# Performance work log

Measured on AMD Instinct MI355X. Metric: run time of the kernel, lower is better.

## Reference

```python
import jax, jax.numpy as jnp
import numpy as np

N = 30000        # entities
R_EFF = 9        # 2*r+1 after enrich() with r=4
F_IN = 256       # insize
HID = 256        # hidden
NCLS = 32        # numcls
BASES = 16
E = 500000       # number of (enriched) triples / nonzeros


def setup_inputs() -> dict:
    key = jax.random.key(0)
    ks = jax.random.split(key, 8)
    features = jax.random.normal(ks[0], (N, F_IN), dtype=jnp.float32)
    # sparse vertical adjacency: entry at (rel*N + dst, src)
    ver_rows = jax.random.randint(ks[1], (E,), 0, R_EFF * N, dtype=jnp.int32)
    ver_cols = jax.random.randint(ks[2], (E,), 0, N, dtype=jnp.int32)
    # row-sum normalization (sum_sparse in the original): vals = 1 / row_degree
    deg = jax.ops.segment_sum(jnp.ones((E,), jnp.float32), ver_rows,
                              num_segments=R_EFF * N)
    ver_vals = 1.0 / deg[ver_rows]
    # xavier-uniform-ish params
    def xavier(k, shape):
        fan_in, fan_out = shape[-2], shape[-1]
        lim = jnp.sqrt(6.0 / (fan_in + fan_out)) * jnp.sqrt(2.0)  # relu gain
        return jax.random.uniform(k, shape, jnp.float32, -lim, lim)
    comps1 = xavier(ks[3], (R_EFF, BASES))
    bases1 = xavier(ks[4], (BASES, F_IN, HID))
    comps2 = xavier(ks[5], (R_EFF, BASES))
    bases2 = xavier(ks[6], (BASES, HID, NCLS))
    bias1 = jnp.zeros((HID,), jnp.float32)
    bias2 = jnp.zeros((NCLS,), jnp.float32)
    return {"features": features, "ver_vals": ver_vals,
            "comps1": comps1, "bases1": bases1,
            "comps2": comps2, "bases2": bases2,
            "bias1": bias1, "bias2": bias2,
            "ver_rows": ver_rows, "ver_cols": ver_cols}


def _spmm(vals, rows, cols, x, num_rows):
    # sparse [num_rows, n] @ x [n, d] -> [num_rows, d]
    msg = vals[:, None] * x[cols]          # (E, d) gather + scale
    return jax.ops.segment_sum(msg, rows, num_segments=num_rows)


def reference(features, ver_vals, comps1, bases1, comps2, bases2,
              bias1, bias2, ver_rows, ver_cols):
    n, f = features.shape
    r = comps1.shape[0]
    # layer 1: sparse aggregate, per-relation transform (basis decomp), sum over r
    h = _spmm(ver_vals, ver_rows, ver_cols, features, r * n)  # (r*n, f)
    h = h.reshape(r, n, f)
    w1 = jnp.einsum('rb,bfe->rfe', comps1, bases1)            # (r, f, hid)
    h = jnp.einsum('rnf,rfe->ne', h, w1)                      # bmm + sum over r
    h = jax.nn.relu(h + bias1)                                # (n, hid)
    # layer 2
    e = h.shape[1]
    h2 = _spmm(ver_vals, ver_rows, ver_cols, h, r * n).reshape(r, n, e)
    w2 = jnp.einsum('rb,bec->rec', comps2, bases2)            # (r, hid, ncls)
    out = jnp.einsum('rne,rec->nc', h2, w2) + bias2           # link_prediction=False
    return out
```

## Files before the change

### kernel.cpp

```cpp
#include <hip/hip_runtime.h>

typedef __attribute__((ext_vector_type(8))) short bf16x8;
typedef __attribute__((ext_vector_type(4))) float f32x4;

constexpr int NB = 16;
constexpr int REFF = 9;

__device__ __forceinline__ unsigned short f2bf(float f) {
  unsigned u = __float_as_uint(f);
  u += 0x7FFFu + ((u >> 16) & 1u);
  return (unsigned short)(u >> 16);
}
__device__ __forceinline__ float bf2f(short s) {
  return __uint_as_float(((unsigned)(unsigned short)s) << 16);
}
__device__ __forceinline__ float bflo(unsigned u) {
  return __uint_as_float(u << 16);
}
__device__ __forceinline__ float bfhi(unsigned u) {
  return __uint_as_float(u & 0xFFFF0000u);
}

__device__ __forceinline__ unsigned short pack_w_one(const float* __restrict__ comps,
                                                     const float* __restrict__ bases,
                                                     int idx, int NTI, int NTOT) {
  int j = idx & 7;
  int lane = (idx >> 3) & 63;
  int ni = (idx >> 9) % NTI;
  int t = (idx >> 9) / NTI;
  int ks = t & 7;
  int r = t >> 3;
  int k = ks * 32 + ((lane >> 4) << 3) + j;
  int n = ni * 16 + (lane & 15);
  float acc = 0.f;
#pragma unroll
  for (int b = 0; b < NB; ++b)
    acc += comps[r * NB + b] * bases[(size_t)b * 256 * NTOT + (size_t)k * NTOT + n];
  return f2bf(acc);
}

__global__ void hist_prep_kernel(const int* __restrict__ rows,
                                 int* __restrict__ deg1, int E,
                                 const float* __restrict__ features,
                                 unsigned short* __restrict__ Xbf,
                                 const float* __restrict__ comps1,
                                 const float* __restrict__ bases1,
                                 unsigned short* __restrict__ W1p,
                                 const float* __restrict__ comps2,
                                 const float* __restrict__ bases2,
                                 unsigned short* __restrict__ W2p, int N) {
  int idx = blockIdx.x * 256 + threadIdx.x;
  if (idx < E) atomicAdd(&deg1[rows[idx]], 1);
  const int n4 = N * 64;
  const int PW1 = REFF * 8 * 16 * 512;
  const int PW2 = REFF * 8 * 2 * 512;
  if (idx < n4) {
    float4 f = reinterpret_cast<const float4*>(features)[idx];
    ushort4 o;
    o.x = f2bf(f.x); o.y = f2bf(f.y); o.z = f2bf(f.z); o.w = f2bf(f.w);
    reinterpret_cast<ushort4*>(Xbf)[idx] = o;
  } else if (idx < n4 + PW1) {
    int i = idx - n4;
    W1p[i] = pack_w_one(comps1, bases1, i, 16, 256);
  } else if (idx < n4 + PW1 + PW2) {
    int i = idx - n4 - PW1;
    W2p[i] = pack_w_one(comps2, bases2, i, 2, 32);
  }
}

__global__ void scan1_kernel(const int* __restrict__ deg, int* __restrict__ bsum,
                             int NR) {
  __shared__ int s[256];
  int t = threadIdx.x;
  int base = blockIdx.x * 1024 + t * 4;
  int acc = 0;
#pragma unroll
  for (int q = 0; q < 4; ++q)
    if (base + q < NR) acc += deg[base + q];
  s[t] = acc;
  __syncthreads();
  for (int off = 128; off > 0; off >>= 1) {
    if (t < off) s[t] += s[t + off];
    __syncthreads();
  }
  if (t == 0) bsum[blockIdx.x] = s[0];
}

__global__ void scan23_kernel(const int* __restrict__ deg,
                              const int* __restrict__ bsum,
                              int* __restrict__ ptr, int NR, int E) {
  __shared__ int s[256];
  __shared__ int sbase;
  int t = threadIdx.x;
  int b = blockIdx.x;
  int part = 0;
  for (int i = t; i < b; i += 256) part += bsum[i];
  s[t] = part;
  __syncthreads();
  for (int off = 128; off > 0; off >>= 1) {
    if (t < off) s[t] += s[t + off];
    __syncthreads();
  }
  if (t == 0) sbase = s[0];
  __syncthreads();
  int base0 = sbase;
  __syncthreads();
  int base = b * 1024 + t * 4;
  int d[4];
#pragma unroll
  for (int q = 0; q < 4; ++q)
    d[q] = (base + q < NR) ? deg[base + q] : 0;
  int tsum = d[0] + d[1] + d[2] + d[3];
  s[t] = tsum;
  __syncthreads();
  for (int off = 1; off < 256; off <<= 1) {
    int x = (t >= off) ? s[t - off] : 0;
    __syncthreads();
    s[t] += x;
    __syncthreads();
  }
  int off0 = base0 + s[t] - tsum;
#pragma unroll
  for (int q = 0; q < 4; ++q) {
    if (base + q < NR) ptr[base + q] = off0;
    off0 += d[q];
  }
  if (b == 0 && t == 0) ptr[NR] = E;
}

__global__ void fill_kernel(const int* __restrict__ rows,
                            const int* __restrict__ cols,
                            int* __restrict__ deg1, const int* __restrict__ ptr1,
                            int* __restrict__ pay1, int E) {
  int e = blockIdx.x * 256 + threadIdx.x;
  if (e >= E) return;
  int g = rows[e];
  int o1 = atomicSub(&deg1[g], 1);
  pay1[ptr1[g] + o1 - 1] = cols[e];
}

__device__ __forceinline__ void gather_row_q(const int* __restrict__ pay,
                                             const int* __restrict__ ptr,
                                             const unsigned short* __restrict__ Xbf,
                                             char* lds, int node0, int N, int r,
                                             int qu, int l16) {
  const int rr = qu;
  const int node = node0 + rr;
  float acc[16];
#pragma unroll
  for (int j = 0; j < 16; ++j) acc[j] = 0.f;
  float s = 0.f;
  if (node < N) {
    int g = r * N + node;
    int p0 = ptr[g], p1 = ptr[g + 1];
    if (p1 > p0) s = 1.0f / (float)(p1 - p0);
    int cnext = 0;
    if (p0 < p1) cnext = pay[p0];
    for (int p = p0; p < p1; ++p) {
      int cc = cnext;
      if (p + 1 < p1) cnext = pay[p + 1];
      const unsigned short* xr = Xbf + (size_t)cc * 256 + l16 * 16;
      bf16x8 x0 = *reinterpret_cast<const bf16x8*>(xr);
      bf16x8 x1 = *reinterpret_cast<const bf16x8*>(xr + 8);
#pragma unroll
      for (int j = 0; j < 8; ++j) {
        acc[j] += bf2f(x0[j]);
        acc[8 + j] += bf2f(x1[j]);
      }
    }
  }
  uint4 o;
  o.x = (unsigned)f2bf(s * acc[0]) | ((unsigned)f2bf(s * acc[1]) << 16);
  o.y = (unsigned)f2bf(s * acc[2]) | ((unsigned)f2bf(s * acc[3]) << 16);
  o.z = (unsigned)f2bf(s * acc[4]) | ((unsigned)f2bf(s * acc[5]) << 16);
  o.w = (unsigned)f2bf(s * acc[6]) | ((unsigned)f2bf(s * acc[7]) << 16);
  *reinterpret_cast<uint4*>(lds + ((rr * 512 + l16 * 32) ^ ((rr & 7) << 4))) = o;
  o.x = (unsigned)f2bf(s * acc[8]) | ((unsigned)f2bf(s * acc[9]) << 16);
  o.y = (unsigned)f2bf(s * acc[10]) | ((unsigned)f2bf(s * acc[11]) << 16);
  o.z = (unsigned)f2bf(s * acc[12]) | ((unsigned)f2bf(s * acc[13]) << 16);
  o.w = (unsigned)f2bf(s * acc[14]) | ((unsigned)f2bf(s * acc[15]) << 16);
  *reinterpret_cast<uint4*>(lds + ((rr * 512 + l16 * 32 + 16) ^ ((rr & 7) << 4))) = o;
}

__global__ __launch_bounds__(512, 8)
void fused_l1(const int* __restrict__ pay1, const int* __restrict__ ptr1,
              const unsigned short* __restrict__ Xbf,
              const unsigned short* __restrict__ W1p,
              const float* __restrict__ bias1,
              const unsigned short* __restrict__ W2p,
              unsigned short* __restrict__ Y2, int N) {
  __shared__ char smem[32 * 1024];
  char* bufA = smem;
  char* bufB = smem + 16 * 1024;
  const int tid = threadIdx.x;
  const int w = tid >> 6, lane = tid & 63;
  const int l15 = lane & 15, kg = lane >> 4;
  const int qu = tid >> 4, l16 = tid & 15;
  const int node0 = blockIdx.x * 32;

  f32x4 acc[2][2];
#pragma unroll
  for (int mi = 0; mi < 2; ++mi)
#pragma unroll
    for (int ni = 0; ni < 2; ++ni) acc[mi][ni] = (f32x4)(0.f);

  gather_row_q(pay1, ptr1, Xbf, bufA, node0, N, 0, qu, l16);
  __syncthreads();

  for (int r = 0; r < REFF; ++r) {
    char* cur = (r & 1) ? bufB : bufA;
    if (r + 1 < REFF) {
      char* nxt = ((r + 1) & 1) ? bufB : bufA;
      gather_row_q(pay1, ptr1, Xbf, nxt, node0, N, r + 1, qu, l16);
    }
#pragma unroll 2
    for (int ks = 0; ks < 8; ++ks) {
      bf16x8 a[2];
#pragma unroll
      for (int mi = 0; mi < 2; ++mi) {
        int row = mi * 16 + l15;
        int boff = (row * 512 + ks * 64 + (kg << 4)) ^ ((row & 7) << 4);
        a[mi] = *reinterpret_cast<const bf16x8*>(cur + boff);
      }
#pragma unroll
      for (int ni = 0; ni < 2; ++ni) {
        int niG = w * 2 + ni;
        bf16x8 b = *reinterpret_cast<const bf16x8*>(
            W1p + (((size_t)(r * 8 + ks) * 16 + niG) << 9) + lane * 8);
#pragma unroll
        for (int mi = 0; mi < 2; ++mi)
          acc[mi][ni] = __builtin_amdgcn_mfma_f32_16x16x32_bf16(a[mi], b,
                                                               acc[mi][ni], 0, 0, 0);
      }
    }
    __syncthreads();
  }

#pragma unroll
  for (int mi = 0; mi < 2; ++mi) {
#pragma unroll
    for (int ni = 0; ni < 2; ++ni) {
      int col = (w * 2 + ni) * 16 + l15;
      float bb = bias1[col];
#pragma unroll
      for (int reg = 0; reg < 4; ++reg) {
        int row = mi * 16 + (kg << 2) + reg;
        float v = fmaxf(acc[mi][ni][reg] + bb, 0.f);
        int b = (row * 512 + col * 2) ^ ((row & 7) << 4);
        *reinterpret_cast<unsigned short*>(bufA + b) = f2bf(v);
      }
    }
  }
  __syncthreads();

  unsigned short* ys = reinterpret_cast<unsigned short*>(bufB) + w * 1024;
  for (int rp = w; rp < REFF; rp += 8) {
    f32x4 a2[2][2];
#pragma unroll
    for (int mi = 0; mi < 2; ++mi) {
      a2[mi][0] = (f32x4)(0.f);
      a2[mi][1] = (f32x4)(0.f);
    }
#pragma unroll
    for (int ks = 0; ks < 8; ++ks) {
      bf16x8 b0 = *reinterpret_cast<const bf16x8*>(
          W2p + (((size_t)(rp * 8 + ks) * 2 + 0) << 9) + lane * 8);
      bf16x8 b1 = *reinterpret_cast<const bf16x8*>(
          W2p + (((size_t)(rp * 8 + ks) * 2 + 1) << 9) + lane * 8);
#pragma unroll
      for (int mi = 0; mi < 2; ++mi) {
        int row = mi * 16 + l15;
        int boff = (row * 512 + ks * 64 + (kg << 4)) ^ ((row & 7) << 4);
        bf16x8 a = *reinterpret_cast<const bf16x8*>(bufA + boff);
        a2[mi][0] = __builtin_amdgcn_mfma_f32_16x16x32_bf16(a, b0, a2[mi][0], 0, 0, 0);
        a2[mi][1] = __builtin_amdgcn_mfma_f32_16x16x32_bf16(a, b1, a2[mi][1], 0, 0, 0);
      }
    }
#pragma unroll
    for (int mi = 0; mi < 2; ++mi)
#pragma unroll
      for (int reg = 0; reg < 4; ++reg) {
        int row16 = mi * 16 + (kg << 2) + reg;
        ys[row16 * 32 + l15] = f2bf(a2[mi][0][reg]);
        ys[row16 * 32 + 16 + l15] = f2bf(a2[mi][1][reg]);
      }
    asm volatile("s_waitcnt lgkmcnt(0)" ::: "memory");
#pragma unroll
    for (int half = 0; half < 2; ++half) {
      int row = half * 16 + (lane >> 2);
      int chunk = lane & 3;
      uint4 v = *reinterpret_cast<const uint4*>(&ys[row * 32 + chunk * 8]);
      int grow = node0 + row;
      if (grow < N)
        *reinterpret_cast<uint4*>(Y2 + (size_t)grow * (REFF * 32) + rp * 32 + chunk * 8) = v;
    }
  }
}

__global__ __launch_bounds__(512, 8)
void gather_out_kernel(const int* __restrict__ pay1,
                       const int* __restrict__ ptr1,
                       const unsigned short* __restrict__ Y2,
                       const float* __restrict__ bias2,
                       float* __restrict__ out, int N) {
  int wv = threadIdx.x >> 6;
  int lane = threadIdx.x & 63;
  int qw = lane >> 4, c = lane & 15;
  int n = blockIdx.x * 8 + wv;
  if (n >= N) return;
  float ax = 0.f, ay = 0.f;
  for (int r = qw; r < REFF; r += 4) {
    int g = r * N + n;
    int p0 = ptr1[g], p1 = ptr1[g + 1];
    if (p0 >= p1) continue;
    float v = 1.0f / (float)(p1 - p0);
    float sx = 0.f, sy = 0.f;
    int p = p0;
    for (; p + 2 <= p1; p += 2) {
      int c0 = pay1[p], c1 = pay1[p + 1];
      unsigned u0 = *reinterpret_cast<const unsigned*>(
          Y2 + (size_t)c0 * (REFF * 32) + r * 32 + c * 2);
      unsigned u1 = *reinterpret_cast<const unsigned*>(
          Y2 + (size_t)c1 * (REFF * 32) + r * 32 + c * 2);
      sx += bflo(u0) + bflo(u1);
      sy += bfhi(u0) + bfhi(u1);
    }
    if (p < p1) {
      int c0 = pay1[p];
      unsigned u0 = *reinterpret_cast<const unsigned*>(
          Y2 + (size_t)c0 * (REFF * 32) + r * 32 + c * 2);
      sx += bflo(u0);
      sy += bfhi(u0);
    }
    ax += v * sx;
    ay += v * sy;
  }
  ax += __shfl_xor(ax, 16); ay += __shfl_xor(ay, 16);
  ax += __shfl_xor(ax, 32); ay += __shfl_xor(ay, 32);
  if (lane < 16) {
    float2 o;
    o.x = ax + bias2[c * 2];
    o.y = ay + bias2[c * 2 + 1];
    reinterpret_cast<float2*>(out)[(size_t)n * 16 + c] = o;
  }
}

extern "C" void kernel_launch(void* const* d_in, const int* in_sizes, int n_in,
                              void* d_out, int out_size, void* d_ws, size_t ws_size,
                              hipStream_t stream) {
  const float* features = (const float*)d_in[0];
  const float* comps1   = (const float*)d_in[2];
  const float* bases1   = (const float*)d_in[3];
  const float* comps2   = (const float*)d_in[4];
  const float* bases2   = (const float*)d_in[5];
  const float* bias1    = (const float*)d_in[6];
  const float* bias2    = (const float*)d_in[7];
  const int* ver_rows   = (const int*)d_in[8];
  const int* ver_cols   = (const int*)d_in[9];

  const int N = in_sizes[0] / 256;
  const int E = in_sizes[1];
  const int NR = REFF * N;
  const int NT = (NR + 1023) / 1024;

  char* p = (char*)d_ws;
  unsigned short* Xbf = (unsigned short*)p; p += (size_t)N * 256 * 2;
  unsigned short* Y2  = (unsigned short*)p; p += (size_t)N * REFF * 32 * 2;
  unsigned short* W1p = (unsigned short*)p; p += (size_t)REFF * 65536 * 2;
  unsigned short* W2p = (unsigned short*)p; p += (size_t)REFF * 8192 * 2;
  int* ptr1 = (int*)p;  p += (size_t)(NR + 4) * 4;
  int* pay1 = (int*)p;  p += (size_t)E * 4;
  int* deg1 = (int*)p;  p += (size_t)NR * 4;
  int* bsum = (int*)p;  p += 512 * 4;

  hipMemsetAsync(deg1, 0, (size_t)NR * 4, stream);
  const int prep_total = N * 64 + REFF * 8 * 16 * 512 + REFF * 8 * 2 * 512;
  const int hp_grid = ((prep_total > E ? prep_total : E) + 255) / 256;
  hist_prep_kernel<<<hp_grid, 256, 0, stream>>>(ver_rows, deg1, E,
                                                features, Xbf,
                                                comps1, bases1, W1p,
                                                comps2, bases2, W2p, N);
  scan1_kernel<<<NT, 256, 0, stream>>>(deg1, bsum, NR);
  scan23_kernel<<<NT, 256, 0, stream>>>(deg1, bsum, ptr1, NR, E);
  fill_kernel<<<(E + 255) / 256, 256, 0, stream>>>(ver_rows, ver_cols,
                                                   deg1, ptr1, pay1, E);

  fused_l1<<<(N + 31) / 32, 512, 0, stream>>>(pay1, ptr1, Xbf, W1p, bias1,
                                              W2p, Y2, N);
  gather_out_kernel<<<(N + 7) / 8, 512, 0, stream>>>(pay1, ptr1, Y2, bias2,
                                                     (float*)d_out, N);
}
```

Before: 195.0 us.

## Remap blocks per XCD, raise MFMA priority, split layer-2 work across waves

Block indices in the fused layer-1 kernel are remapped so that consecutive node tiles land on the same XCD, which should improve L2 locality for neighbouring nodes. MFMA loops are wrapped in s_setprio to favour compute waves over waves issuing gathers. The layer-2 projection now splits each relation into two 16-row halves, giving 18 work items across the 8 waves instead of 9. That balances wave load better, but each wave reloads the W2 fragments once per half.

```diff
diff --git a/kernel.cpp b/kernel.cpp
--- a/kernel.cpp
+++ b/kernel.cpp
@@ -5,6 +5,7 @@
 
 constexpr int NB = 16;
 constexpr int REFF = 9;
+constexpr int NXCD = 8;
 
 __device__ __forceinline__ unsigned short f2bf(float f) {
   unsigned u = __float_as_uint(f);
@@ -188,7 +189,7 @@
               const unsigned short* __restrict__ W1p,
               const float* __restrict__ bias1,
               const unsigned short* __restrict__ W2p,
-              unsigned short* __restrict__ Y2, int N) {
+              unsigned short* __restrict__ Y2, int N, int nwg) {
   __shared__ char smem[32 * 1024];
   char* bufA = smem;
   char* bufB = smem + 16 * 1024;
@@ -196,7 +197,14 @@
   const int w = tid >> 6, lane = tid & 63;
   const int l15 = lane & 15, kg = lane >> 4;
   const int qu = tid >> 4, l16 = tid & 15;
-  const int node0 = blockIdx.x * 32;
+
+  int bid;
+  {
+    int q = nwg / NXCD, rem = nwg % NXCD;
+    int xcd = blockIdx.x % NXCD, idx = blockIdx.x / NXCD;
+    bid = (xcd < rem ? xcd * (q + 1) : rem * (q + 1) + (xcd - rem) * q) + idx;
+  }
+  const int node0 = bid * 32;
 
   f32x4 acc[2][2];
 #pragma unroll
@@ -213,6 +221,7 @@
       char* nxt = ((r + 1) & 1) ? bufB : bufA;
       gather_row_q(pay1, ptr1, Xbf, nxt, node0, N, r + 1, qu, l16);
     }
+    __builtin_amdgcn_s_setprio(1);
 #pragma unroll 2
     for (int ks = 0; ks < 8; ++ks) {
       bf16x8 a[2];
@@ -233,6 +242,7 @@
                                                                acc[mi][ni], 0, 0, 0);
       }
     }
+    __builtin_amdgcn_s_setprio(0);
     __syncthreads();
   }
 
@@ -254,43 +264,37 @@
   __syncthreads();
 
   unsigned short* ys = reinterpret_cast<unsigned short*>(bufB) + w * 1024;
-  for (int rp = w; rp < REFF; rp += 8) {
-    f32x4 a2[2][2];
-#pragma unroll
-    for (int mi = 0; mi < 2; ++mi) {
-      a2[mi][0] = (f32x4)(0.f);
-      a2[mi][1] = (f32x4)(0.f);
-    }
+  for (int j = w; j < 18; j += 8) {
+    int rp = j >> 1, mih = j & 1;
+    f32x4 a2[2];
+    a2[0] = (f32x4)(0.f);
+    a2[1] = (f32x4)(0.f);
+    __builtin_amdgcn_s_setprio(1);
 #pragma unroll
     for (int ks = 0; ks < 8; ++ks) {
       bf16x8 b0 = *reinterpret_cast<const bf16x8*>(
           W2p + (((size_t)(rp * 8 + ks) * 2 + 0) << 9) + lane * 8);
       bf16x8 b1 = *reinterpret_cast<const bf16x8*>(
           W2p + (((size_t)(rp * 8 + ks) * 2 + 1) << 9) + lane * 8);
-#pragma unroll
-      for (int mi = 0; mi < 2; ++mi) {
-        int row = mi * 16 + l15;
-        int boff = (row * 512 + ks * 64 + (kg << 4)) ^ ((row & 7) << 4);
-        bf16x8 a = *reinterpret_cast<const bf16x8*>(bufA + boff);
-        a2[mi][0] = __builtin_amdgcn_mfma_f32_16x16x32_bf16(a, b0, a2[mi][0], 0, 0, 0);
-        a2[mi][1] = __builtin_amdgcn_mfma_f32_16x16x32_bf16(a, b1, a2[mi][1], 0, 0, 0);
-      }
-    }
-#pragma unroll
-    for (int mi = 0; mi < 2; ++mi)
-#pragma unroll
-      for (int reg = 0; reg < 4; ++reg) {
-        int row16 = mi * 16 + (kg << 2) + reg;
-        ys[row16 * 32 + l15] = f2bf(a2[mi][0][reg]);
-        ys[row16 * 32 + 16 + l15] = f2bf(a2[mi][1][reg]);
-      }
+      int row = mih * 16 + l15;
+      int boff = (row * 512 + ks * 64 + (kg << 4)) ^ ((row & 7) << 4);
+      bf16x8 a = *reinterpret_cast<const bf16x8*>(bufA + boff);
+      a2[0] = __builtin_amdgcn_mfma_f32_16x16x32_bf16(a, b0, a2[0], 0, 0, 0);
+      a2[1] = __builtin_amdgcn_mfma_f32_16x16x32_bf16(a, b1, a2[1], 0, 0, 0);
+    }
+    __builtin_amdgcn_s_setprio(0);
+#pragma unroll
+    for (int reg = 0; reg < 4; ++reg) {
+      int row16 = (kg << 2) + reg;
+      ys[row16 * 32 + l15] = f2bf(a2[0][reg]);
+      ys[row16 * 32 + 16 + l15] = f2bf(a2[1][reg]);
+    }
     asm volatile("s_waitcnt lgkmcnt(0)" ::: "memory");
-#pragma unroll
-    for (int half = 0; half < 2; ++half) {
-      int row = half * 16 + (lane >> 2);
+    {
+      int row = lane >> 2;
       int chunk = lane & 3;
       uint4 v = *reinterpret_cast<const uint4*>(&ys[row * 32 + chunk * 8]);
-      int grow = node0 + row;
+      int grow = node0 + mih * 16 + row;
       if (grow < N)
         *reinterpret_cast<uint4*>(Y2 + (size_t)grow * (REFF * 32) + rp * 32 + chunk * 8) = v;
     }
@@ -385,8 +389,9 @@
   fill_kernel<<<(E + 255) / 256, 256, 0, stream>>>(ver_rows, ver_cols,
                                                    deg1, ptr1, pay1, E);
 
-  fused_l1<<<(N + 31) / 32, 512, 0, stream>>>(pay1, ptr1, Xbf, W1p, bias1,
-                                              W2p, Y2, N);
+  const int nwg = (N + 31) / 32;
+  fused_l1<<<nwg, 512, 0, stream>>>(pay1, ptr1, Xbf, W1p, bias1,
+                                    W2p, Y2, N, nwg);
   gather_out_kernel<<<(N + 7) / 8, 512, 0, stream>>>(pay1, ptr1, Y2, bias2,
                                                      (float*)d_out, N);
 }
```

Measured after the change: 185.1 us. -5.1%, faster.
